# Kernel optimization log

Hardware: AMD Instinct MI355X
Metric: run time of the kernel (lower is better)

## Reference

```python
import jax, jax.numpy as jnp
import numpy as np

D_MODEL = 1024
N_HEADS = 16
D_K = D_MODEL // N_HEADS


def setup_inputs() -> dict:
    key = jax.random.key(0)
    ks = jax.random.split(key, 12)
    B, S, D, H = 2, 2048, D_MODEL, N_HEADS
    s = 1.0 / np.sqrt(D)
    inp = {
        "x": jax.random.normal(ks[0], (B, S, D), jnp.float32),
        "Wq": jax.random.normal(ks[1], (D, D), jnp.float32) * s,
        "bq": jnp.zeros((D,), jnp.float32),
        "Wk": jax.random.normal(ks[2], (D, D), jnp.float32) * s,
        "bk": jnp.zeros((D,), jnp.float32),
        "Wv": jax.random.normal(ks[3], (D, D), jnp.float32) * s,
        "bv": jnp.zeros((D,), jnp.float32),
        "Wo": jax.random.normal(ks[4], (D, D), jnp.float32) * s,
        "bo": jnp.zeros((D,), jnp.float32),
        "Wp": jax.random.normal(ks[5], (D, H), jnp.float32) * s,
        "bp": jnp.zeros((H,), jnp.float32),
        "alpha": jax.random.normal(ks[6], (H,), jnp.float32) * 0.1,
    }
    return inp


def reference(x, Wq, bq, Wk, bk, Wv, bv, Wo, bo, Wp, bp, alpha):
    B, S, D = x.shape
    H, dk = N_HEADS, D_K
    scale = dk ** -0.5
    # projections -> (B, H, S, dk)
    Q = (x @ Wq + bq).reshape(B, S, H, dk).transpose(0, 2, 1, 3)
    K = (x @ Wk + bk).reshape(B, S, H, dk).transpose(0, 2, 1, 3)
    V = (x @ Wv + bv).reshape(B, S, H, dk).transpose(0, 2, 1, 3)
    scores = jnp.einsum("bhid,bhjd->bhij", Q, K) * scale  # (B,H,S,S)
    # phase derived from x: (B,S,H) -> (B,H,S)
    phase = (x @ Wp + bp).transpose(0, 2, 1)
    # coherence(i,j) = cos(phi_i - phi_j), per batch/head
    coherence = jnp.cos(phase[:, :, :, None] - phase[:, :, None, :])
    scores = scores + alpha[None, :, None, None] * coherence
    attn = jax.nn.softmax(scores, axis=-1)
    out = jnp.einsum("bhij,bhjd->bhid", attn, V)  # (B,H,S,dk)
    out = out.transpose(0, 2, 1, 3).reshape(B, S, D)
    return out @ Wo + bo
```

## Files before the change

### kernel.cpp

```cpp
#include <hip/hip_runtime.h>
#include <math.h>


#define S_LEN 2048
#define NHEADS 16

typedef __attribute__((ext_vector_type(8))) short short8;
typedef __attribute__((ext_vector_type(4))) float floatx4;
typedef __attribute__((ext_vector_type(2))) float float2v;
typedef __attribute__((ext_vector_type(4))) unsigned int uintx4;

__device__ inline unsigned short f2bf(float f) {
    union { float f; unsigned int i; } v; v.f = f;
    unsigned int u = v.i;
    return (unsigned short)((u + 0x7fffu + ((u >> 16) & 1u)) >> 16);
}
__device__ inline unsigned int pack2_bf16(float hi, float lo) {
    union { float f; unsigned int u; } a, b; a.f = hi; b.f = lo;
    return __builtin_amdgcn_perm(a.u, b.u, 0x07060302u);
}
__device__ inline void async_copy16(const unsigned short* src, unsigned short* dst_lds) {
    __builtin_amdgcn_global_load_lds(
        (const __attribute__((address_space(1))) unsigned int*)(src),
        (__attribute__((address_space(3))) unsigned int*)(dst_lds), 16, 0, 0);
}

__global__ __launch_bounds__(256) void prep_kernel(
    const float* __restrict__ x, const float* __restrict__ Wp,
    const float* __restrict__ bp,
    const float* __restrict__ w0, const float* __restrict__ w1,
    const float* __restrict__ w2, const float* __restrict__ w3,
    unsigned short* __restrict__ d0, unsigned short* __restrict__ d1,
    unsigned short* __restrict__ d2, unsigned short* __restrict__ d3,
    float* __restrict__ cosP, float* __restrict__ sinP,
    unsigned short* __restrict__ xb) {
    __shared__ __align__(16) unsigned short shmem[64 * 72];
    int t = threadIdx.x;
    if (blockIdx.x < 4096) {
        float* fb = reinterpret_cast<float*>(shmem);
        float* xs = fb;
        float4* red4 = reinterpret_cast<float4*>(fb + 1024);
        int bid = blockIdx.x;
        int b = bid >> 11, s = bid & 2047;
        const float* xr = x + (size_t)bid * 1024;
        float4 xv = *reinterpret_cast<const float4*>(&xr[t * 4]);
        {
            uint2 o;
            o.x = (unsigned int)f2bf(xv.x) | ((unsigned int)f2bf(xv.y) << 16);
            o.y = (unsigned int)f2bf(xv.z) | ((unsigned int)f2bf(xv.w) << 16);
            *reinterpret_cast<uint2*>(&xb[(size_t)bid * 1024 + t * 4]) = o;
        }
        *reinterpret_cast<float4*>(&xs[t * 4]) = xv;
        __syncthreads();
        float f0 = 0.f, f1 = 0.f, f2 = 0.f, f3 = 0.f;
        int krow = t >> 2;
        const float4* wp4 = reinterpret_cast<const float4*>(Wp);
#pragma unroll
        for (int i = 0; i < 16; i++) {
            float4 wv = wp4[i * 256 + t];
            float xk = xs[i * 64 + krow];
            f0 += xk * wv.x; f1 += xk * wv.y; f2 += xk * wv.z; f3 += xk * wv.w;
        }
        red4[t] = make_float4(f0, f1, f2, f3);
        __syncthreads();
        if (t < 16) {
            int b2 = t >> 2, comp = t & 3;
            const float* rf = fb + 1024;
            float sum = bp[t];
#pragma unroll
            for (int j = 0; j < 64; j++) sum += rf[(4 * j + b2) * 4 + comp];
            float sv, cv;
            __sincosf(sum, &sv, &cv);
            size_t o = ((size_t)b * NHEADS + t) * S_LEN + s;
            cosP[o] = cv; sinP[o] = sv;
        }
    } else {
        unsigned short (*tile)[72] = reinterpret_cast<unsigned short (*)[72]>(shmem);
        int bid = blockIdx.x - 4096;
        int mat = bid >> 8;
        int tl  = bid & 255;
        int tr = tl >> 4, tc = tl & 15;
        const float* src    = (mat == 0) ? w0 : (mat == 1) ? w1 : (mat == 2) ? w2 : w3;
        unsigned short* dst = (mat == 0) ? d0 : (mat == 1) ? d1 : (mat == 2) ? d2 : d3;
        int col = t & 63, rbase = (t >> 6) * 16;
#pragma unroll
        for (int i = 0; i < 16; i++) {
            int row = rbase + i;
            tile[row][col] = f2bf(src[(size_t)(tr * 64 + row) * 1024 + tc * 64 + col]);
        }
        __syncthreads();
#pragma unroll
        for (int i = 0; i < 16; i++) {
            int row = rbase + i;
            dst[(size_t)(tc * 64 + row) * 1024 + tr * 64 + col] = tile[col][row];
        }
    }
}

template <int MT>
__global__ __launch_bounds__(256) void gemm_bt(
    const unsigned short* __restrict__ A, const unsigned short* __restrict__ BT,
    int N, int mode,
    const float* __restrict__ b0, const float* __restrict__ b1,
    const float* __restrict__ b2,
    unsigned short* __restrict__ o0, unsigned short* __restrict__ o1,
    unsigned short* __restrict__ o2, float* __restrict__ of) {
    __shared__ __align__(16) unsigned short As[MT * 32];
    __shared__ __align__(16) unsigned short Bs[128 * 32];
    const int K = 1024;
    const int MI = MT / 32;
    int t = threadIdx.x;
    int mBase = blockIdx.x * MT;
    int nBase = blockIdx.y * 128;
    int w = t >> 6, lane = t & 63, l15 = lane & 15, quad = lane >> 4;
    int wm = (w & 1) * (MT / 2), wn = (w >> 1) * 64;
    floatx4 acc[MI][4];
#pragma unroll
    for (int i = 0; i < MI; i++)
#pragma unroll
        for (int j = 0; j < 4; j++) acc[i][j] = (floatx4){0.f, 0.f, 0.f, 0.f};

    int arow = t >> 2, aseg = (t & 3) * 8;
    for (int k0 = 0; k0 < K; k0 += 32) {
        __syncthreads();
#pragma unroll
        for (int i = 0; i < MT / 64; i++)
            async_copy16(&A[(size_t)(mBase + i * 64 + arow) * K + k0 + aseg],
                         &As[(i * 64 + arow) * 32 + aseg]);
#pragma unroll
        for (int i = 0; i < 2; i++)
            async_copy16(&BT[(size_t)(nBase + i * 64 + arow) * K + k0 + aseg],
                         &Bs[(i * 64 + arow) * 32 + aseg]);
        __syncthreads();
        short8 af[MI], bfr[4];
#pragma unroll
        for (int mi = 0; mi < MI; mi++)
            af[mi] = *reinterpret_cast<const short8*>(&As[(wm + mi * 16 + l15) * 32 + quad * 8]);
#pragma unroll
        for (int ni = 0; ni < 4; ni++)
            bfr[ni] = *reinterpret_cast<const short8*>(&Bs[(wn + ni * 16 + l15) * 32 + quad * 8]);
#pragma unroll
        for (int mi = 0; mi < MI; mi++)
#pragma unroll
            for (int ni = 0; ni < 4; ni++)
                acc[mi][ni] = __builtin_amdgcn_mfma_f32_16x16x32_bf16(af[mi], bfr[ni], acc[mi][ni], 0, 0, 0);
    }

#pragma unroll
    for (int mi = 0; mi < MI; mi++) {
        int rowB = mBase + wm + mi * 16 + quad * 4;
#pragma unroll
        for (int ni = 0; ni < 4; ni++) {
            int col = nBase + wn + ni * 16 + l15;
            if (mode == 0) {
                float bias = b0[col];
#pragma unroll
                for (int r = 0; r < 4; r++) {
                    of[(size_t)(rowB + r) * N + col] = acc[mi][ni][r] + bias;
                }
            } else {
                int mat = col >> 10, nn = col & 1023;
                int h = nn >> 6, d = nn & 63;
                int b = rowB >> 11, sidx = rowB & 2047;
                if (mat == 2) {
                    float bv = b2[nn];
                    int jj = sidx & 63;
                    size_t rowOff = ((size_t)((b * NHEADS + h) * 64 + d)) * S_LEN +
                                    (sidx & ~63);
#pragma unroll
                    for (int r = 0; r < 4; r++) {
                        int j2 = jj + r;
                        int u = 4 * (j2 & 15) + (j2 >> 4);
                        o2[rowOff + u] = f2bf(acc[mi][ni][r] + bv);
                    }
                } else {
                    const float* bias  = (mat == 0) ? b0 : b1;
                    unsigned short* op = (mat == 0) ? o0 : o1;
                    float bv = bias[nn];
                    float scl = (mat == 0) ? 0.18033688f : 1.0f;
#pragma unroll
                    for (int r = 0; r < 4; r++) {
                        float cv = (acc[mi][ni][r] + bv) * scl;
                        op[(((size_t)b * NHEADS + h) * S_LEN + (sidx + r)) * 64 + d] = f2bf(cv);
                    }
                }
            }
        }
    }
}

__global__ __launch_bounds__(1024) void attn_kernel(
    const unsigned short* __restrict__ Qg, const unsigned short* __restrict__ Kg,
    const unsigned short* __restrict__ VTg,
    const float* __restrict__ cosP, const float* __restrict__ sinP,
    const float* __restrict__ alpha, unsigned short* __restrict__ ctx) {
    __shared__ __align__(16) unsigned short KsB[2][64 * 64];
    __shared__ __align__(16) unsigned short VtB[2][64 * 64];
    __shared__ __align__(16) unsigned short Plb[16][16 * 72];

    int x = blockIdx.x;
    int bh = (x & 7) * 4 + (x >> 6);
    int qt = (x >> 3) & 7;
    int t = threadIdx.x, w = t >> 6, lane = t & 63, l15 = lane & 15, quad = lane >> 4;
    int m0 = qt * 256 + w * 16;
    size_t base = (size_t)bh * (S_LEN * 64);
    size_t phBase = (size_t)bh * S_LEN;
    const float L2E = 1.44269504f;

    int th = t & 511;
    int sj = th >> 3, sg = th & 7;
    int srot = ((sg - (sj & 7)) & 7) * 8;
    bool stK = (t < 512);

    short8 qf[2];
#pragma unroll
    for (int c = 0; c < 2; c++)
        qf[c] = *reinterpret_cast<const short8*>(
            &Qg[base + (size_t)(m0 + l15) * 64 + c * 32 + quad * 8]);

    float alph = alpha[bh & 15] * L2E;
    float2v ci2[2], si2[2];
#pragma unroll
    for (int hh = 0; hh < 2; hh++) {
        size_t o = phBase + m0 + quad * 4 + hh * 2;
        ci2[hh] = (float2v){alph * cosP[o], alph * cosP[o + 1]};
        si2[hh] = (float2v){alph * sinP[o], alph * sinP[o + 1]};
    }

    {
        if (stK) async_copy16(&Kg[base + (size_t)sj * 64 + srot], &KsB[0][th * 8]);
        else     async_copy16(&VTg[base + (size_t)sj * S_LEN + srot], &VtB[0][th * 8]);
    }

    floatx4 oacc[4], lacc;
#pragma unroll
    for (int tt = 0; tt < 4; tt++) oacc[tt] = (floatx4){0.f, 0.f, 0.f, 0.f};
    lacc = (floatx4){0.f, 0.f, 0.f, 0.f};
    const short8 ones8 = {(short)0x3F80, (short)0x3F80, (short)0x3F80, (short)0x3F80,
                          (short)0x3F80, (short)0x3F80, (short)0x3F80, (short)0x3F80};

    int rot = l15 & 7;
    int cb0 = 16 * ((quad + rot) & 7);
    int cb1 = 16 * ((quad + 4 + rot) & 7);

    for (int kt = 0; kt < 32; kt++) {
        int p = kt & 1;
        __syncthreads();
        if (kt < 31) {
            int kn = kt + 1, pn = p ^ 1;
            if (stK) async_copy16(&Kg[base + (size_t)(kn * 64 + sj) * 64 + srot], &KsB[pn][th * 8]);
            else     async_copy16(&VTg[base + (size_t)sj * S_LEN + kn * 64 + srot], &VtB[pn][th * 8]);
        }

        float cjv[4], sjv[4];
        {
            const float* cpb = &cosP[phBase + kt * 64];
            const float* spb = &sinP[phBase + kt * 64];
#pragma unroll
            for (int jt = 0; jt < 4; jt++) {
                cjv[jt] = cpb[jt * 16 + l15];
                sjv[jt] = spb[jt * 16 + l15];
            }
        }

        floatx4 st[4];
#pragma unroll
        for (int jt = 0; jt < 4; jt++) {
            const char* kr = (const char*)&KsB[p][(jt * 16 + l15) * 64];
            short8 kf0 = *reinterpret_cast<const short8*>(kr + cb0);
            short8 kf1 = *reinterpret_cast<const short8*>(kr + cb1);
            floatx4 s = (floatx4){0.f, 0.f, 0.f, 0.f};
            s = __builtin_amdgcn_mfma_f32_16x16x32_bf16(qf[0], kf0, s, 0, 0, 0);
            s = __builtin_amdgcn_mfma_f32_16x16x32_bf16(qf[1], kf1, s, 0, 0, 0);
            st[jt] = s;
        }

        uint2* pl2 = reinterpret_cast<uint2*>(&Plb[w][0]);
#pragma unroll
        for (int rp = 0; rp < 2; rp++) {
            float2v a0, a1, a2, a3;
            {
                float2v s0 = (float2v){st[0][rp * 2], st[0][rp * 2 + 1]};
                float2v s1 = (float2v){st[1][rp * 2], st[1][rp * 2 + 1]};
                float2v s2 = (float2v){st[2][rp * 2], st[2][rp * 2 + 1]};
                float2v s3 = (float2v){st[3][rp * 2], st[3][rp * 2 + 1]};
                a0 = si2[rp] * sjv[0] + (ci2[rp] * cjv[0] + s0);
                a1 = si2[rp] * sjv[1] + (ci2[rp] * cjv[1] + s1);
                a2 = si2[rp] * sjv[2] + (ci2[rp] * cjv[2] + s2);
                a3 = si2[rp] * sjv[3] + (ci2[rp] * cjv[3] + s3);
            }
            int row = quad * 4 + rp * 2;
            {
                uint2 o;
                o.x = pack2_bf16(__builtin_amdgcn_exp2f(a1.x), __builtin_amdgcn_exp2f(a0.x));
                o.y = pack2_bf16(__builtin_amdgcn_exp2f(a3.x), __builtin_amdgcn_exp2f(a2.x));
                pl2[row * 18 + l15] = o;
            }
            {
                uint2 o;
                o.x = pack2_bf16(__builtin_amdgcn_exp2f(a1.y), __builtin_amdgcn_exp2f(a0.y));
                o.y = pack2_bf16(__builtin_amdgcn_exp2f(a3.y), __builtin_amdgcn_exp2f(a2.y));
                pl2[(row + 1) * 18 + l15] = o;
            }
        }

        short8 pf[2];
#pragma unroll
        for (int c = 0; c < 2; c++)
            pf[c] = *reinterpret_cast<const short8*>(
                &Plb[w][l15 * 72 + c * 32 + quad * 8]);

#pragma unroll
        for (int c = 0; c < 2; c++) {
            int cb = c ? cb1 : cb0;
#pragma unroll
            for (int tt = 0; tt < 4; tt++) {
                const char* vr = (const char*)&VtB[p][(tt * 16 + l15) * 64];
                short8 vf = *reinterpret_cast<const short8*>(vr + cb);
                oacc[tt] = __builtin_amdgcn_mfma_f32_16x16x32_bf16(pf[c], vf, oacc[tt], 0, 0, 0);
            }
            lacc = __builtin_amdgcn_mfma_f32_16x16x32_bf16(pf[c], ones8, lacc, 0, 0, 0);
        }
    }

    int b = bh >> 4, h = bh & 15;
    float inv[4];
#pragma unroll
    for (int r = 0; r < 4; r++) inv[r] = 1.0f / lacc[r];
#pragma unroll
    for (int tt = 0; tt < 4; tt++)
#pragma unroll
        for (int r = 0; r < 4; r++) {
            int srow = m0 + quad * 4 + r;
            ctx[((size_t)(b * S_LEN + srow)) * 1024 + h * 64 + tt * 16 + l15] =
                f2bf(oacc[tt][r] * inv[r]);
        }
}

extern "C" void kernel_launch(void* const* d_in, const int* in_sizes, int n_in,
                              void* d_out, int out_size, void* d_ws, size_t ws_size,
                              hipStream_t stream) {
    const float* x     = (const float*)d_in[0];
    const float* Wq    = (const float*)d_in[1];
    const float* bq    = (const float*)d_in[2];
    const float* Wk    = (const float*)d_in[3];
    const float* bk    = (const float*)d_in[4];
    const float* Wv    = (const float*)d_in[5];
    const float* bv    = (const float*)d_in[6];
    const float* Wo    = (const float*)d_in[7];
    const float* bo    = (const float*)d_in[8];
    const float* Wp    = (const float*)d_in[9];
    const float* bp    = (const float*)d_in[10];
    const float* alpha = (const float*)d_in[11];
    float* out = (float*)d_out;

    const size_t MB = 1048576;
    char* ws = (char*)d_ws;
    unsigned short* WT   = (unsigned short*)(ws);
    unsigned short* WoT  = (unsigned short*)(ws + 6 * MB);
    unsigned short* xb   = (unsigned short*)(ws + 8 * MB);
    unsigned short* ctx  = (unsigned short*)(ws + 8 * MB);
    unsigned short* Qw   = (unsigned short*)(ws + 16 * MB);
    unsigned short* Kw   = (unsigned short*)(ws + 24 * MB);
    unsigned short* VTg  = (unsigned short*)(ws + 32 * MB);
    float* cosP          = (float*)(ws + 40 * MB);
    float* sinP          = (float*)(ws + 40 * MB + 262144);

    prep_kernel<<<dim3(5120), dim3(256), 0, stream>>>(
        x, Wp, bp, Wq, Wk, Wv, Wo,
        WT, WT + 1048576, WT + 2097152, WoT, cosP, sinP, xb);
    gemm_bt<128><<<dim3(32, 24), dim3(256), 0, stream>>>(
        xb, WT, 3072, 1, bq, bk, bv, Qw, Kw, VTg, (float*)nullptr);
    attn_kernel<<<dim3(256), dim3(1024), 0, stream>>>(
        Qw, Kw, VTg, cosP, sinP, alpha, ctx);
    gemm_bt<64><<<dim3(64, 8), dim3(256), 0, stream>>>(
        ctx, WoT, 1024, 0, bo, bo, bo,
        (unsigned short*)nullptr, (unsigned short*)nullptr,
        (unsigned short*)nullptr, out);
}
```

Before: 218.4 us.

## Keep softmax probabilities in registers by transposing QK MFMA and permuting V layout

Swaps the MFMA operand order so each lane receives the score values for its own query row, with keys along the accumulator dimension. The probabilities can then be packed straight into the bf16 A-operand for the PV MFMA, with no round trip through shared memory. The V-transpose layout written by the projection kernel is permuted so that the key ordering matches the packed register fragment. This removes the per-wave LDS buffer along with its stores and loads, in exchange for a more intricate layout coupling between the two kernels and per-iteration float4 loads of the cos/sin phase values.

```diff
diff --git a/kernel.cpp b/kernel.cpp
--- a/kernel.cpp
+++ b/kernel.cpp
@@ -8,7 +8,6 @@
 typedef __attribute__((ext_vector_type(8))) short short8;
 typedef __attribute__((ext_vector_type(4))) float floatx4;
 typedef __attribute__((ext_vector_type(2))) float float2v;
-typedef __attribute__((ext_vector_type(4))) unsigned int uintx4;
 
 __device__ inline unsigned short f2bf(float f) {
     union { float f; unsigned int i; } v; v.f = f;
@@ -170,7 +169,8 @@
 #pragma unroll
                     for (int r = 0; r < 4; r++) {
                         int j2 = jj + r;
-                        int u = 4 * (j2 & 15) + (j2 >> 4);
+                        int jt = j2 >> 4;
+                        int u = (jt >> 1) * 32 + ((j2 & 15) >> 2) * 8 + (jt & 1) * 4 + (j2 & 3);
                         o2[rowOff + u] = f2bf(acc[mi][ni][r] + bv);
                     }
                 } else {
@@ -196,7 +196,6 @@
     const float* __restrict__ alpha, unsigned short* __restrict__ ctx) {
     __shared__ __align__(16) unsigned short KsB[2][64 * 64];
     __shared__ __align__(16) unsigned short VtB[2][64 * 64];
-    __shared__ __align__(16) unsigned short Plb[16][16 * 72];
 
     int x = blockIdx.x;
     int bh = (x & 7) * 4 + (x >> 6);
@@ -219,13 +218,9 @@
             &Qg[base + (size_t)(m0 + l15) * 64 + c * 32 + quad * 8]);
 
     float alph = alpha[bh & 15] * L2E;
-    float2v ci2[2], si2[2];
-#pragma unroll
-    for (int hh = 0; hh < 2; hh++) {
-        size_t o = phBase + m0 + quad * 4 + hh * 2;
-        ci2[hh] = (float2v){alph * cosP[o], alph * cosP[o + 1]};
-        si2[hh] = (float2v){alph * sinP[o], alph * sinP[o + 1]};
-    }
+    float ci = alph * cosP[phBase + m0 + l15];
+    float si = alph * sinP[phBase + m0 + l15];
+    float2v ci2 = (float2v){ci, ci}, si2 = (float2v){si, si};
 
     {
         if (stK) async_copy16(&Kg[base + (size_t)sj * 64 + srot], &KsB[0][th * 8]);
@@ -250,17 +245,6 @@
             int kn = kt + 1, pn = p ^ 1;
             if (stK) async_copy16(&Kg[base + (size_t)(kn * 64 + sj) * 64 + srot], &KsB[pn][th * 8]);
             else     async_copy16(&VTg[base + (size_t)sj * S_LEN + kn * 64 + srot], &VtB[pn][th * 8]);
-        }
-
-        float cjv[4], sjv[4];
-        {
-            const float* cpb = &cosP[phBase + kt * 64];
-            const float* spb = &sinP[phBase + kt * 64];
-#pragma unroll
-            for (int jt = 0; jt < 4; jt++) {
-                cjv[jt] = cpb[jt * 16 + l15];
-                sjv[jt] = spb[jt * 16 + l15];
-            }
         }
 
         floatx4 st[4];
@@ -270,56 +254,46 @@
             short8 kf0 = *reinterpret_cast<const short8*>(kr + cb0);
             short8 kf1 = *reinterpret_cast<const short8*>(kr + cb1);
             floatx4 s = (floatx4){0.f, 0.f, 0.f, 0.f};
-            s = __builtin_amdgcn_mfma_f32_16x16x32_bf16(qf[0], kf0, s, 0, 0, 0);
-            s = __builtin_amdgcn_mfma_f32_16x16x32_bf16(qf[1], kf1, s, 0, 0, 0);
+            s = __builtin_amdgcn_mfma_f32_16x16x32_bf16(kf0, qf[0], s, 0, 0, 0);
+            s = __builtin_amdgcn_mfma_f32_16x16x32_bf16(kf1, qf[1], s, 0, 0, 0);
             st[jt] = s;
         }
 
-        uint2* pl2 = reinterpret_cast<uint2*>(&Plb[w][0]);
-#pragma unroll
-        for (int rp = 0; rp < 2; rp++) {
-            float2v a0, a1, a2, a3;
-            {
-                float2v s0 = (float2v){st[0][rp * 2], st[0][rp * 2 + 1]};
-                float2v s1 = (float2v){st[1][rp * 2], st[1][rp * 2 + 1]};
-                float2v s2 = (float2v){st[2][rp * 2], st[2][rp * 2 + 1]};
-                float2v s3 = (float2v){st[3][rp * 2], st[3][rp * 2 + 1]};
-                a0 = si2[rp] * sjv[0] + (ci2[rp] * cjv[0] + s0);
-                a1 = si2[rp] * sjv[1] + (ci2[rp] * cjv[1] + s1);
-                a2 = si2[rp] * sjv[2] + (ci2[rp] * cjv[2] + s2);
-                a3 = si2[rp] * sjv[3] + (ci2[rp] * cjv[3] + s3);
-            }
-            int row = quad * 4 + rp * 2;
-            {
-                uint2 o;
-                o.x = pack2_bf16(__builtin_amdgcn_exp2f(a1.x), __builtin_amdgcn_exp2f(a0.x));
-                o.y = pack2_bf16(__builtin_amdgcn_exp2f(a3.x), __builtin_amdgcn_exp2f(a2.x));
-                pl2[row * 18 + l15] = o;
-            }
-            {
-                uint2 o;
-                o.x = pack2_bf16(__builtin_amdgcn_exp2f(a1.y), __builtin_amdgcn_exp2f(a0.y));
-                o.y = pack2_bf16(__builtin_amdgcn_exp2f(a3.y), __builtin_amdgcn_exp2f(a2.y));
-                pl2[(row + 1) * 18 + l15] = o;
-            }
-        }
-
-        short8 pf[2];
-#pragma unroll
-        for (int c = 0; c < 2; c++)
-            pf[c] = *reinterpret_cast<const short8*>(
-                &Plb[w][l15 * 72 + c * 32 + quad * 8]);
+        union PW { unsigned int u[4]; short8 s8; };
+        PW P0, P1;
+#pragma unroll
+        for (int jt = 0; jt < 4; jt++) {
+            const float* cpb = &cosP[phBase + kt * 64 + jt * 16 + quad * 4];
+            const float* spb = &sinP[phBase + kt * 64 + jt * 16 + quad * 4];
+            float4 cj = *reinterpret_cast<const float4*>(cpb);
+            float4 sjv = *reinterpret_cast<const float4*>(spb);
+            float2v st01 = (float2v){st[jt][0], st[jt][1]};
+            float2v st23 = (float2v){st[jt][2], st[jt][3]};
+            float2v c01 = (float2v){cj.x, cj.y}, c23 = (float2v){cj.z, cj.w};
+            float2v s01 = (float2v){sjv.x, sjv.y}, s23 = (float2v){sjv.z, sjv.w};
+            float2v a01 = si2 * s01 + (ci2 * c01 + st01);
+            float2v a23 = si2 * s23 + (ci2 * c23 + st23);
+            unsigned int wA = pack2_bf16(__builtin_amdgcn_exp2f(a01.y),
+                                         __builtin_amdgcn_exp2f(a01.x));
+            unsigned int wB = pack2_bf16(__builtin_amdgcn_exp2f(a23.y),
+                                         __builtin_amdgcn_exp2f(a23.x));
+            if (jt == 0)      { P0.u[0] = wA; P0.u[1] = wB; }
+            else if (jt == 1) { P0.u[2] = wA; P0.u[3] = wB; }
+            else if (jt == 2) { P1.u[0] = wA; P1.u[1] = wB; }
+            else              { P1.u[2] = wA; P1.u[3] = wB; }
+        }
 
 #pragma unroll
         for (int c = 0; c < 2; c++) {
+            short8 pf = c ? P1.s8 : P0.s8;
             int cb = c ? cb1 : cb0;
 #pragma unroll
             for (int tt = 0; tt < 4; tt++) {
                 const char* vr = (const char*)&VtB[p][(tt * 16 + l15) * 64];
                 short8 vf = *reinterpret_cast<const short8*>(vr + cb);
-                oacc[tt] = __builtin_amdgcn_mfma_f32_16x16x32_bf16(pf[c], vf, oacc[tt], 0, 0, 0);
+                oacc[tt] = __builtin_amdgcn_mfma_f32_16x16x32_bf16(pf, vf, oacc[tt], 0, 0, 0);
             }
-            lacc = __builtin_amdgcn_mfma_f32_16x16x32_bf16(pf[c], ones8, lacc, 0, 0, 0);
+            lacc = __builtin_amdgcn_mfma_f32_16x16x32_bf16(pf, ones8, lacc, 0, 0, 0);
         }
     }
 
```

After: 242.2 us. 1.11x slower.
